# Optimization experiments

Hardware: AMD Instinct MI355X
Metric: run time of the kernel (lower is better)

Reference implementation:

```python
import jax, jax.numpy as jnp
import numpy as np

DIM = 384
DEPTH = 4
HEADS = 6
DIM_HEAD = 64
INNER = HEADS * DIM_HEAD  # 384
MLP = 1536
B, N = 4, 2048


def setup_inputs() -> dict:
    key = jax.random.key(0)
    ks = jax.random.split(key, 7)
    s = 0.02
    x = jax.random.normal(ks[0], (B, N, DIM), dtype=jnp.float32)
    Wqkv = jax.random.normal(ks[1], (DEPTH, DIM, 3 * INNER), dtype=jnp.float32) * s
    Wout = jax.random.normal(ks[2], (DEPTH, INNER, DIM), dtype=jnp.float32) * s
    W1 = jax.random.normal(ks[3], (DEPTH, DIM, MLP), dtype=jnp.float32) * s
    b1 = jax.random.normal(ks[4], (DEPTH, MLP), dtype=jnp.float32) * s
    W2 = jax.random.normal(ks[5], (DEPTH, MLP, DIM), dtype=jnp.float32) * s
    b2 = jax.random.normal(ks[6], (DEPTH, DIM), dtype=jnp.float32) * s
    return {"x": x, "Wqkv": Wqkv, "Wout": Wout, "W1": W1, "b1": b1, "W2": W2, "b2": b2}


def _attention(x, Wqkv_l, Wout_l):
    scale = DIM_HEAD ** (-0.5)
    qkv = jnp.einsum('bnd,de->bne', x, Wqkv_l)  # [B,N,3*INNER]
    q, k, v = jnp.split(qkv, 3, axis=-1)
    # [B,N,INNER] -> [B,H,N,Dh]
    reshape = lambda t: t.reshape(B, N, HEADS, DIM_HEAD).transpose(0, 2, 1, 3)
    q, k, v = reshape(q), reshape(k), reshape(v)
    dots = jnp.einsum('bhnd,bhmd->bhnm', q, k) * scale
    attn = jax.nn.softmax(dots, axis=-1)
    out = jnp.einsum('bhnm,bhmd->bhnd', attn, v)
    out = out.transpose(0, 2, 1, 3).reshape(B, N, INNER)
    return jnp.einsum('bne,ed->bnd', out, Wout_l)


def _ff(x, W1_l, b1_l, W2_l, b2_l):
    h = jax.nn.gelu(jnp.einsum('bnd,dh->bnh', x, W1_l) + b1_l, approximate=False)
    return jnp.einsum('bnh,hd->bnd', h, W2_l) + b2_l


def reference(x, Wqkv, Wout, W1, b1, W2, b2):
    for l in range(DEPTH):
        x = _attention(x, Wqkv[l], Wout[l]) + x
        x = _ff(x, W1[l], b1[l], W2[l], b2[l]) + x
    return x
```

## Files before the change

kernel.cpp:

```cpp
#include <hip/hip_runtime.h>
#include <stdint.h>

#define HEADS 6
#define NN 2048
#define BB 4
#define MTOT (BB*NN)
#define DEPTH 4

typedef unsigned short u16;
typedef __attribute__((ext_vector_type(8))) short bf16x8;
typedef __attribute__((ext_vector_type(4))) float f32x4;
typedef __attribute__((ext_vector_type(16))) float f32x16;

#define MFMA32(a,b,c) __builtin_amdgcn_mfma_f32_32x32x16_bf16((a),(b),(c),0,0,0)

#define QSC 0.18033688011112042f

__device__ __forceinline__ u16 f2bf(float f) {
  union { float f; uint32_t u; } v; v.f = f;
  uint32_t r = v.u + 0x7fffu + ((v.u >> 16) & 1u);
  return (u16)(r >> 16);
}

__device__ __forceinline__ uint32_t pk2(float lo, float hi) {
  uint32_t r;
  asm("v_cvt_pk_bf16_f32 %0, %1, %2" : "=v"(r) : "v"(lo), "v"(hi));
  return r;
}

__device__ __forceinline__ void gload_lds16(const void* g, void* l) {
  __builtin_amdgcn_global_load_lds((const __attribute__((address_space(1))) void*)g,
                                   (__attribute__((address_space(3))) void*)l, 16, 0, 0);
}

__global__ __launch_bounds__(256)
void wtrans_k(const float* __restrict__ in, u16* __restrict__ out, int K, int N) {
  __shared__ float t[32][33];
  const int z = blockIdx.z;
  in  += (size_t)z * K * N;
  out += (size_t)z * K * N;
  const int n0 = blockIdx.x * 32, k0 = blockIdx.y * 32;
  const int tx = threadIdx.x & 31, ty = threadIdx.x >> 5;
#pragma unroll
  for (int i = 0; i < 4; ++i)
    t[ty + i*8][tx] = in[(size_t)(k0 + ty + i*8) * N + n0 + tx];
  __syncthreads();
#pragma unroll
  for (int i = 0; i < 4; ++i)
    out[(size_t)(n0 + ty + i*8) * K + k0 + tx] = f2bf(t[tx][ty + i*8]);
}

__global__ __launch_bounds__(256)
void xprep_k(const float* __restrict__ x, u16* __restrict__ xbf, int n) {
  int i = blockIdx.x * 256 + threadIdx.x;
  if (i < n) xbf[i] = f2bf(x[i]);
}

template<int MODE>
__global__ __launch_bounds__(256)
void gemm64_k(const u16* __restrict__ A, const u16* __restrict__ Bt,
              const float* __restrict__ bias, const float* __restrict__ res,
              float* __restrict__ outF, u16* __restrict__ outB,
              u16* __restrict__ qb, u16* __restrict__ kb, u16* __restrict__ vtb,
              int M, int N, int K) {
  __shared__ u16 smA[64 * 64];
  __shared__ u16 smB[64 * 64];
  const int tid = threadIdx.x;
  const int lane = tid & 63, wv = tid >> 6;
  const int wr = wv >> 1, wc = wv & 1;
  const int l31 = lane & 31, h2 = lane >> 5;
  const int row0 = blockIdx.y * 64, col0 = blockIdx.x * 64;

  f32x16 acc;
#pragma unroll
  for (int i = 0; i < 16; ++i) acc[i] = 0.f;

  const int c0 = tid, c1 = tid + 256;
  const int r0 = c0 >> 3, s0 = (c0 & 7) ^ (r0 & 7);
  const int r1 = c1 >> 3, s1 = (c1 & 7) ^ (r1 & 7);

  const int ksteps = K >> 6;
  for (int kt = 0; kt < ksteps; ++kt) {
    const int k0 = kt << 6;
    const u16* Ab = A  + (size_t)row0 * K + k0;
    const u16* Bb = Bt + (size_t)col0 * K + k0;
    gload_lds16(Ab + (size_t)r0 * K + s0 * 8, smA + wv * 512);
    gload_lds16(Ab + (size_t)r1 * K + s1 * 8, smA + 2048 + wv * 512);
    gload_lds16(Bb + (size_t)r0 * K + s0 * 8, smB + wv * 512);
    gload_lds16(Bb + (size_t)r1 * K + s1 * 8, smB + 2048 + wv * 512);
    __syncthreads();
    const int ra = wr * 32 + l31;
    const int rb = wc * 32 + l31;
#pragma unroll
    for (int ks = 0; ks < 4; ++ks) {
      bf16x8 af = *(const bf16x8*)(smA + ra * 64 + (((ks * 2 + h2) ^ (ra & 7)) * 8));
      bf16x8 bf = *(const bf16x8*)(smB + rb * 64 + (((ks * 2 + h2) ^ (rb & 7)) * 8));
      acc = MFMA32(af, bf, acc);
    }
    __syncthreads();
  }

  const int col = col0 + wc * 32 + l31;
  if (MODE == 0) {
    const int sec = col / 384, c3 = col - sec * 384;
    const int hh = c3 >> 6, d = c3 & 63;
#pragma unroll
    for (int c = 0; c < 4; ++c)
#pragma unroll
      for (int j = 0; j < 4; ++j) {
        const int row = row0 + wr * 32 + 8 * c + 4 * h2 + j;
        const int bb = row >> 11, n = row & 2047;
        const float v = acc[4 * c + j];
        if (sec == 0)       qb [(((size_t)bb * HEADS + hh) * NN + n) * 64 + d] = f2bf(v * QSC);
        else if (sec == 1)  kb [(((size_t)bb * HEADS + hh) * NN + n) * 64 + d] = f2bf(v);
        else                vtb[(((size_t)bb * HEADS + hh) * 64 + d) * NN + n] = f2bf(v);
      }
  } else {
#pragma unroll
    for (int c = 0; c < 4; ++c)
#pragma unroll
      for (int j = 0; j < 4; ++j) {
        const int row = row0 + wr * 32 + 8 * c + 4 * h2 + j;
        float v = acc[4 * c + j];
        if (MODE == 1) {
          size_t idx = (size_t)row * N + col;
          v += res[idx];
          outF[idx] = v;
          outB[idx] = f2bf(v);
        } else if (MODE == 2) {
          v += bias[col];
          v = 0.5f * v * (1.0f + erff(v * 0.70710678118f));
          outB[(size_t)row * N + col] = f2bf(v);
        } else {
          size_t idx = (size_t)row * N + col;
          v += bias[col] + res[idx];
          outF[idx] = v;
          outB[idx] = f2bf(v);
        }
      }
  }
}

__global__ __launch_bounds__(128)
void attn_k(const u16* __restrict__ qb, const u16* __restrict__ kb,
            const u16* __restrict__ vtb, u16* __restrict__ ob) {
  __shared__ u16 kb3[3][64 * 64];
  __shared__ u16 vb3[3][64 * 64];
  const int tid = threadIdx.x;
  const int lane = tid & 63, wv = tid >> 6;
  const int l31 = lane & 31, h2 = lane >> 5;
  const int qx = l31 & 7;

  const int lid = blockIdx.y * 32 + blockIdx.x;
  const int xcd = lid & 7, ii = lid >> 3;
  const int bh = 3 * xcd + (ii >> 5);
  const int qblk = ii & 31;
  const int b = bh / HEADS, h = bh - b * HEADS;
  const int q0 = qblk * 64 + wv * 32;

  const u16* Qb = qb + ((size_t)bh * NN + q0 + l31) * 64;
  bf16x8 qf[4];
#pragma unroll
  for (int ct2 = 0; ct2 < 4; ++ct2)
    qf[ct2] = *(const bf16x8*)(Qb + ct2 * 16 + h2 * 8);

  float m = -1e30f, s = 0.f;
  f32x16 acc[2];
#pragma unroll
  for (int dg = 0; dg < 2; ++dg)
#pragma unroll
    for (int i = 0; i < 16; ++i) acc[dg][i] = 0.f;
  const f32x16 zero16 = {0.f,0.f,0.f,0.f,0.f,0.f,0.f,0.f,0.f,0.f,0.f,0.f,0.f,0.f,0.f,0.f};

  const u16* Kb0 = kb  + (size_t)bh * NN * 64;
  const u16* Vt0 = vtb + (size_t)bh * 64 * NN;
  int rr[4], ss[4];
#pragma unroll
  for (int k = 0; k < 4; ++k) {
    const int c = wv * 64 + lane + k * 128;
    rr[k] = c >> 3;
    ss[k] = (c & 7) ^ (rr[k] & 7);
  }

#define STAGE3(kd, vd, t) do { \
    _Pragma("unroll") \
    for (int k = 0; k < 4; ++k) { \
      gload_lds16(Kb0 + (size_t)(t) * 4096 + (size_t)rr[k] * 64 + ss[k] * 8, \
                  (kd) + wv * 512 + k * 1024); \
      gload_lds16(Vt0 + (size_t)rr[k] * NN + (t) * 64 + ss[k] * 8, \
                  (vd) + wv * 512 + k * 1024); \
    } \
  } while (0)

  u16 *kA = kb3[0], *kB = kb3[1], *kC = kb3[2];
  u16 *vA = vb3[0], *vB = vb3[1], *vC = vb3[2];

  STAGE3(kA, vA, 0);
  __syncthreads();

  bf16x8 pf[4];
  const int NT = NN / 64;
  for (int kt = 0; kt < NT; ++kt) {
    if (kt + 1 < NT) STAGE3(kB, vB, kt + 1);

    f32x16 st[2];
#pragma unroll
    for (int kg = 0; kg < 2; ++kg) {
      f32x16 a = zero16;
      const u16* krow = kA + (kg * 32 + l31) * 64;
#pragma unroll
      for (int ct2 = 0; ct2 < 4; ++ct2) {
        bf16x8 kf = *(const bf16x8*)(krow + ((ct2 * 2 + h2) ^ qx) * 8);
        a = MFMA32(kf, qf[ct2], a);
      }
      st[kg] = a;
    }
    if (kt > 0) {
#pragma unroll
      for (int kgp = 0; kgp < 4; ++kgp)
#pragma unroll
        for (int dg = 0; dg < 2; ++dg) {
          const int d = dg * 32 + l31;
          bf16x8 vf = *(const bf16x8*)(vC + d * 64 + (((kgp * 2 + h2) ^ (d & 7)) * 8));
          acc[dg] = MFMA32(vf, pf[kgp], acc[dg]);
        }
    }

    float tmax = -1e30f;
#pragma unroll
    for (int kg = 0; kg < 2; ++kg)
#pragma unroll
      for (int i = 0; i < 16; ++i) tmax = fmaxf(tmax, st[kg][i]);
    if (!__all(tmax <= m + 8.0f)) {
      float rm = fmaxf(tmax, __shfl_xor(tmax, 32));
      float mn = fmaxf(m, rm);
      float al = __builtin_amdgcn_exp2f(m - mn);
      s *= al;
#pragma unroll
      for (int dg = 0; dg < 2; ++dg)
#pragma unroll
        for (int i = 0; i < 16; ++i) acc[dg][i] *= al;
      m = mn;
    }
    float p[2][16];
    float r = 0.f;
#pragma unroll
    for (int kg = 0; kg < 2; ++kg)
#pragma unroll
      for (int i = 0; i < 16; ++i) {
        float t = __builtin_amdgcn_exp2f(st[kg][i] - m);
        p[kg][i] = t;
        r += t;
      }
    r += __shfl_xor(r, 32);
    s += r;

#pragma unroll
    for (int kg = 0; kg < 2; ++kg)
#pragma unroll
      for (int sub = 0; sub < 2; ++sub) {
        const int s8 = sub * 8;
        uint32_t X0 = pk2(p[kg][s8 + 0], p[kg][s8 + 1]);
        uint32_t X1 = pk2(p[kg][s8 + 2], p[kg][s8 + 3]);
        uint32_t Y0 = pk2(p[kg][s8 + 4], p[kg][s8 + 5]);
        uint32_t Y1 = pk2(p[kg][s8 + 6], p[kg][s8 + 7]);
        asm volatile("v_permlane32_swap_b32 %0, %1" : "+v"(X0), "+v"(Y0));
        asm volatile("v_permlane32_swap_b32 %0, %1" : "+v"(X1), "+v"(Y1));
        union { uint32_t u[4]; bf16x8 v; } pu;
        pu.u[0] = X0; pu.u[1] = X1; pu.u[2] = Y0; pu.u[3] = Y1;
        pf[kg * 2 + sub] = pu.v;
      }

    __syncthreads();
    u16* t1 = kA; kA = kB; kB = kC; kC = t1;
    u16* t2 = vA; vA = vB; vB = vC; vC = t2;
  }

#pragma unroll
  for (int kgp = 0; kgp < 4; ++kgp)
#pragma unroll
    for (int dg = 0; dg < 2; ++dg) {
      const int d = dg * 32 + l31;
      bf16x8 vf = *(const bf16x8*)(vC + d * 64 + (((kgp * 2 + h2) ^ (d & 7)) * 8));
      acc[dg] = MFMA32(vf, pf[kgp], acc[dg]);
    }

  const float inv = 1.f / s;
  u16* orow = ob + ((size_t)b * NN + q0 + l31) * 384 + h * 64;
#pragma unroll
  for (int dg = 0; dg < 2; ++dg)
#pragma unroll
    for (int c = 0; c < 4; ++c) {
      uint2 w;
      w.x = pk2(acc[dg][4*c + 0] * inv, acc[dg][4*c + 1] * inv);
      w.y = pk2(acc[dg][4*c + 2] * inv, acc[dg][4*c + 3] * inv);
      *(uint2*)(orow + dg * 32 + 8 * c + 4 * h2) = w;
    }
}

extern "C" void kernel_launch(void* const* d_in, const int* in_sizes, int n_in,
                              void* d_out, int out_size, void* d_ws, size_t ws_size,
                              hipStream_t stream) {
  (void)in_sizes; (void)n_in; (void)out_size; (void)ws_size;
  const float* x    = (const float*)d_in[0];
  const float* Wqkv = (const float*)d_in[1];
  const float* Wout = (const float*)d_in[2];
  const float* W1   = (const float*)d_in[3];
  const float* b1   = (const float*)d_in[4];
  const float* W2   = (const float*)d_in[5];
  const float* b2   = (const float*)d_in[6];
  float* out = (float*)d_out;

  char* ws = (char*)d_ws;
  size_t off = 0;
  auto alloc = [&](size_t bytes) { char* p = ws + off; off += (bytes + 255) & ~(size_t)255; return p; };
  u16*   wqkvT = (u16*)alloc((size_t)DEPTH * 1152 * 384 * 2);
  u16*   woutT = (u16*)alloc((size_t)DEPTH * 384 * 384 * 2);
  u16*   w1T   = (u16*)alloc((size_t)DEPTH * 1536 * 384 * 2);
  u16*   w2T   = (u16*)alloc((size_t)DEPTH * 384 * 1536 * 2);
  u16*   xbf   = (u16*)alloc((size_t)MTOT * 384 * 2);
  float* xres  = (float*)alloc((size_t)MTOT * 384 * 4);
  u16*   qbuf  = (u16*)alloc((size_t)MTOT * 384 * 2);
  u16*   kbuf  = (u16*)alloc((size_t)MTOT * 384 * 2);
  u16*   vtbuf = (u16*)alloc((size_t)MTOT * 384 * 2);
  u16*   obuf  = (u16*)alloc((size_t)MTOT * 384 * 2);
  u16*   hbuf  = (u16*)alloc((size_t)MTOT * 1536 * 2);

  wtrans_k<<<dim3(1152/32, 384/32, DEPTH), 256, 0, stream>>>(Wqkv, wqkvT, 384, 1152);
  wtrans_k<<<dim3( 384/32, 384/32, DEPTH), 256, 0, stream>>>(Wout, woutT, 384, 384);
  wtrans_k<<<dim3(1536/32, 384/32, DEPTH), 256, 0, stream>>>(W1,   w1T,   384, 1536);
  wtrans_k<<<dim3( 384/32,1536/32, DEPTH), 256, 0, stream>>>(W2,   w2T,   1536, 384);
  xprep_k<<<(MTOT*384 + 255)/256, 256, 0, stream>>>(x, xbf, MTOT*384);

  for (int l = 0; l < DEPTH; ++l) {
    gemm64_k<0><<<dim3(1152/64, MTOT/64), 256, 0, stream>>>(
        xbf, wqkvT + (size_t)l*1152*384, nullptr, nullptr, nullptr, nullptr,
        qbuf, kbuf, vtbuf, MTOT, 1152, 384);
    attn_k<<<dim3(32, 24), 128, 0, stream>>>(qbuf, kbuf, vtbuf, obuf);
    gemm64_k<1><<<dim3(384/64, MTOT/64), 256, 0, stream>>>(
        obuf, woutT + (size_t)l*384*384, nullptr, (l == 0 ? x : xres), xres, xbf,
        nullptr, nullptr, nullptr, MTOT, 384, 384);
    gemm64_k<2><<<dim3(1536/64, MTOT/64), 256, 0, stream>>>(
        xbf, w1T + (size_t)l*1536*384, b1 + l*1536, nullptr, nullptr, hbuf,
        nullptr, nullptr, nullptr, MTOT, 1536, 384);
    gemm64_k<3><<<dim3(384/64, MTOT/64), 256, 0, stream>>>(
        hbuf, w2T + (size_t)l*384*1536, b2 + l*384, xres,
        (l == DEPTH-1 ? out : xres), xbf,
        nullptr, nullptr, nullptr, MTOT, 384, 1536);
  }
}
```

Baseline: 582.8 us.

## Split attention KV sequence across two wave pairs and merge partial softmax

Attention blocks now use 256 threads: two wave pairs each process half of the key/value sequence (split-K flash attention) with 32-key tiles, then the second pair writes its partial accumulators, max and sum to shared memory and the first pair merges them with rescaling before writing output. This doubles waves per block, aiming to raise occupancy and latency hiding on a grid of only 768 blocks. It adds a shared-memory merge step, a final barrier, and smaller per-iteration MFMA work, which may add loop overhead.

New measurement: 539.4 us. 7.4% less time.

```diff
diff --git a/kernel.cpp b/kernel.cpp
--- a/kernel.cpp
+++ b/kernel.cpp
@@ -141,22 +141,23 @@
   }
 }
 
-__global__ __launch_bounds__(128)
+__global__ __launch_bounds__(256)
 void attn_k(const u16* __restrict__ qb, const u16* __restrict__ kb,
             const u16* __restrict__ vtb, u16* __restrict__ ob) {
-  __shared__ u16 kb3[3][64 * 64];
-  __shared__ u16 vb3[3][64 * 64];
+  __shared__ u16 kb3[3][2][32 * 64];
+  __shared__ u16 vb3[3][2][64 * 32];
   const int tid = threadIdx.x;
   const int lane = tid & 63, wv = tid >> 6;
   const int l31 = lane & 31, h2 = lane >> 5;
-  const int qx = l31 & 7;
+  const int hs = wv >> 1;
+  const int qg = wv & 1;
 
   const int lid = blockIdx.y * 32 + blockIdx.x;
   const int xcd = lid & 7, ii = lid >> 3;
   const int bh = 3 * xcd + (ii >> 5);
   const int qblk = ii & 31;
   const int b = bh / HEADS, h = bh - b * HEADS;
-  const int q0 = qblk * 64 + wv * 32;
+  const int q0 = qblk * 64 + qg * 32;
 
   const u16* Qb = qb + ((size_t)bh * NN + q0 + l31) * 64;
   bf16x8 qf[4];
@@ -174,63 +175,53 @@
 
   const u16* Kb0 = kb  + (size_t)bh * NN * 64;
   const u16* Vt0 = vtb + (size_t)bh * 64 * NN;
-  int rr[4], ss[4];
-#pragma unroll
-  for (int k = 0; k < 4; ++k) {
-    const int c = wv * 64 + lane + k * 128;
-    rr[k] = c >> 3;
-    ss[k] = (c & 7) ^ (rr[k] & 7);
-  }
+  const int rK = tid >> 3, sK = (tid & 7) ^ (rK & 7);
+  const int rV = tid >> 2, sV = (tid & 3) ^ (rV & 3);
 
 #define STAGE3(kd, vd, t) do { \
     _Pragma("unroll") \
-    for (int k = 0; k < 4; ++k) { \
-      gload_lds16(Kb0 + (size_t)(t) * 4096 + (size_t)rr[k] * 64 + ss[k] * 8, \
-                  (kd) + wv * 512 + k * 1024); \
-      gload_lds16(Vt0 + (size_t)rr[k] * NN + (t) * 64 + ss[k] * 8, \
-                  (vd) + wv * 512 + k * 1024); \
+    for (int hf = 0; hf < 2; ++hf) { \
+      gload_lds16(Kb0 + ((size_t)(hf * 1024 + (t) * 32 + rK)) * 64 + sK * 8, \
+                  (kd) + hf * 2048 + wv * 512); \
+      gload_lds16(Vt0 + (size_t)rV * NN + hf * 1024 + (t) * 32 + sV * 8, \
+                  (vd) + hf * 2048 + wv * 512); \
     } \
   } while (0)
 
-  u16 *kA = kb3[0], *kB = kb3[1], *kC = kb3[2];
-  u16 *vA = vb3[0], *vB = vb3[1], *vC = vb3[2];
+  u16 *kA = &kb3[0][0][0], *kB = &kb3[1][0][0], *kC = &kb3[2][0][0];
+  u16 *vA = &vb3[0][0][0], *vB = &vb3[1][0][0], *vC = &vb3[2][0][0];
 
   STAGE3(kA, vA, 0);
   __syncthreads();
 
-  bf16x8 pf[4];
-  const int NT = NN / 64;
+  bf16x8 pf[2];
+  const int NT = 1024 / 32;
   for (int kt = 0; kt < NT; ++kt) {
     if (kt + 1 < NT) STAGE3(kB, vB, kt + 1);
 
-    f32x16 st[2];
-#pragma unroll
-    for (int kg = 0; kg < 2; ++kg) {
-      f32x16 a = zero16;
-      const u16* krow = kA + (kg * 32 + l31) * 64;
+    f32x16 st = zero16;
+    {
+      const u16* krow = kA + hs * 2048 + l31 * 64;
 #pragma unroll
       for (int ct2 = 0; ct2 < 4; ++ct2) {
-        bf16x8 kf = *(const bf16x8*)(krow + ((ct2 * 2 + h2) ^ qx) * 8);
-        a = MFMA32(kf, qf[ct2], a);
+        bf16x8 kf = *(const bf16x8*)(krow + (((ct2 * 2 + h2) ^ (l31 & 7)) * 8));
+        st = MFMA32(kf, qf[ct2], st);
       }
-      st[kg] = a;
     }
     if (kt > 0) {
 #pragma unroll
-      for (int kgp = 0; kgp < 4; ++kgp)
+      for (int ks = 0; ks < 2; ++ks)
 #pragma unroll
         for (int dg = 0; dg < 2; ++dg) {
           const int d = dg * 32 + l31;
-          bf16x8 vf = *(const bf16x8*)(vC + d * 64 + (((kgp * 2 + h2) ^ (d & 7)) * 8));
-          acc[dg] = MFMA32(vf, pf[kgp], acc[dg]);
+          bf16x8 vf = *(const bf16x8*)(vC + hs * 2048 + d * 32 + (((ks * 2 + h2) ^ (d & 3)) * 8));
+          acc[dg] = MFMA32(vf, pf[ks], acc[dg]);
         }
     }
 
     float tmax = -1e30f;
 #pragma unroll
-    for (int kg = 0; kg < 2; ++kg)
-#pragma unroll
-      for (int i = 0; i < 16; ++i) tmax = fmaxf(tmax, st[kg][i]);
+    for (int i = 0; i < 16; ++i) tmax = fmaxf(tmax, st[i]);
     if (!__all(tmax <= m + 8.0f)) {
       float rm = fmaxf(tmax, __shfl_xor(tmax, 32));
       float mn = fmaxf(m, rm);
@@ -242,34 +233,30 @@
         for (int i = 0; i < 16; ++i) acc[dg][i] *= al;
       m = mn;
     }
-    float p[2][16];
+    float p[16];
     float r = 0.f;
 #pragma unroll
-    for (int kg = 0; kg < 2; ++kg)
-#pragma unroll
-      for (int i = 0; i < 16; ++i) {
-        float t = __builtin_amdgcn_exp2f(st[kg][i] - m);
-        p[kg][i] = t;
-        r += t;
-      }
+    for (int i = 0; i < 16; ++i) {
+      float t = __builtin_amdgcn_exp2f(st[i] - m);
+      p[i] = t;
+      r += t;
+    }
     r += __shfl_xor(r, 32);
     s += r;
 
 #pragma unroll
-    for (int kg = 0; kg < 2; ++kg)
-#pragma unroll
-      for (int sub = 0; sub < 2; ++sub) {
-        const int s8 = sub * 8;
-        uint32_t X0 = pk2(p[kg][s8 + 0], p[kg][s8 + 1]);
-        uint32_t X1 = pk2(p[kg][s8 + 2], p[kg][s8 + 3]);
-        uint32_t Y0 = pk2(p[kg][s8 + 4], p[kg][s8 + 5]);
-        uint32_t Y1 = pk2(p[kg][s8 + 6], p[kg][s8 + 7]);
-        asm volatile("v_permlane32_swap_b32 %0, %1" : "+v"(X0), "+v"(Y0));
-        asm volatile("v_permlane32_swap_b32 %0, %1" : "+v"(X1), "+v"(Y1));
-        union { uint32_t u[4]; bf16x8 v; } pu;
-        pu.u[0] = X0; pu.u[1] = X1; pu.u[2] = Y0; pu.u[3] = Y1;
-        pf[kg * 2 + sub] = pu.v;
-      }
+    for (int sub = 0; sub < 2; ++sub) {
+      const int s8 = sub * 8;
+      uint32_t X0 = pk2(p[s8 + 0], p[s8 + 1]);
+      uint32_t X1 = pk2(p[s8 + 2], p[s8 + 3]);
+      uint32_t Y0 = pk2(p[s8 + 4], p[s8 + 5]);
+      uint32_t Y1 = pk2(p[s8 + 6], p[s8 + 7]);
+      asm volatile("v_permlane32_swap_b32 %0, %1" : "+v"(X0), "+v"(Y0));
+      asm volatile("v_permlane32_swap_b32 %0, %1" : "+v"(X1), "+v"(Y1));
+      union { uint32_t u[4]; bf16x8 v; } pu;
+      pu.u[0] = X0; pu.u[1] = X1; pu.u[2] = Y0; pu.u[3] = Y1;
+      pf[sub] = pu.v;
+    }
 
     __syncthreads();
     u16* t1 = kA; kA = kB; kB = kC; kC = t1;
@@ -277,25 +264,47 @@
   }
 
 #pragma unroll
-  for (int kgp = 0; kgp < 4; ++kgp)
+  for (int ks = 0; ks < 2; ++ks)
 #pragma unroll
     for (int dg = 0; dg < 2; ++dg) {
       const int d = dg * 32 + l31;
-      bf16x8 vf = *(const bf16x8*)(vC + d * 64 + (((kgp * 2 + h2) ^ (d & 7)) * 8));
-      acc[dg] = MFMA32(vf, pf[kgp], acc[dg]);
-    }
-
-  const float inv = 1.f / s;
-  u16* orow = ob + ((size_t)b * NN + q0 + l31) * 384 + h * 64;
-#pragma unroll
-  for (int dg = 0; dg < 2; ++dg)
-#pragma unroll
-    for (int c = 0; c < 4; ++c) {
-      uint2 w;
-      w.x = pk2(acc[dg][4*c + 0] * inv, acc[dg][4*c + 1] * inv);
-      w.y = pk2(acc[dg][4*c + 2] * inv, acc[dg][4*c + 3] * inv);
-      *(uint2*)(orow + dg * 32 + 8 * c + 4 * h2) = w;
-    }
+      bf16x8 vf = *(const bf16x8*)(vC + hs * 2048 + d * 32 + (((ks * 2 + h2) ^ (d & 3)) * 8));
+      acc[dg] = MFMA32(vf, pf[ks], acc[dg]);
+    }
+
+  float* mb = (float*)kb3;
+  if (wv >= 2) {
+    const int base = ((wv - 2) * 64 + lane) * 36;
+#pragma unroll
+    for (int dg = 0; dg < 2; ++dg)
+#pragma unroll
+      for (int i = 0; i < 16; ++i) mb[base + dg * 16 + i] = acc[dg][i];
+    mb[base + 32] = m;
+    mb[base + 33] = s;
+  }
+  __syncthreads();
+  if (wv < 2) {
+    const int base = (wv * 64 + lane) * 36;
+    const float m2 = mb[base + 32], s2 = mb[base + 33];
+    const float M  = fmaxf(m, m2);
+    const float a1 = __builtin_amdgcn_exp2f(m  - M);
+    const float a2 = __builtin_amdgcn_exp2f(m2 - M);
+    const float inv = 1.f / (s * a1 + s2 * a2);
+    u16* orow = ob + ((size_t)b * NN + q0 + l31) * 384 + h * 64;
+#pragma unroll
+    for (int dg = 0; dg < 2; ++dg)
+#pragma unroll
+      for (int c = 0; c < 4; ++c) {
+        float v0 = (acc[dg][4*c + 0] * a1 + mb[base + dg*16 + 4*c + 0] * a2) * inv;
+        float v1 = (acc[dg][4*c + 1] * a1 + mb[base + dg*16 + 4*c + 1] * a2) * inv;
+        float v2 = (acc[dg][4*c + 2] * a1 + mb[base + dg*16 + 4*c + 2] * a2) * inv;
+        float v3 = (acc[dg][4*c + 3] * a1 + mb[base + dg*16 + 4*c + 3] * a2) * inv;
+        uint2 w;
+        w.x = pk2(v0, v1);
+        w.y = pk2(v2, v3);
+        *(uint2*)(orow + dg * 32 + 8 * c + 4 * h2) = w;
+      }
+  }
 }
 
 extern "C" void kernel_launch(void* const* d_in, const int* in_sizes, int n_in,
@@ -336,7 +345,7 @@
     gemm64_k<0><<<dim3(1152/64, MTOT/64), 256, 0, stream>>>(
         xbf, wqkvT + (size_t)l*1152*384, nullptr, nullptr, nullptr, nullptr,
         qbuf, kbuf, vtbuf, MTOT, 1152, 384);
-    attn_k<<<dim3(32, 24), 128, 0, stream>>>(qbuf, kbuf, vtbuf, obuf);
+    attn_k<<<dim3(32, 24), 256, 0, stream>>>(qbuf, kbuf, vtbuf, obuf);
     gemm64_k<1><<<dim3(384/64, MTOT/64), 256, 0, stream>>>(
         obuf, woutT + (size_t)l*384*384, nullptr, (l == 0 ? x : xres), xres, xbf,
         nullptr, nullptr, nullptr, MTOT, 384, 384);
```
